# Optimization experiments

Measured on AMD Instinct MI355X. Metric: run time of the kernel, lower is better.

Reference implementation:

```python
import jax, jax.numpy as jnp
import numpy as np

INPUT_DIM = 1024
EMBED_DIM = 1024

def setup_inputs() -> dict:
    key = jax.random.key(0)
    ks = jax.random.split(key, 6)
    B, S = 4, 2048
    q = jax.random.normal(ks[0], (B, S, INPUT_DIM), dtype=jnp.float32)
    k = jax.random.normal(ks[1], (B, S, INPUT_DIM), dtype=jnp.float32)
    v = jax.random.normal(ks[2], (B, S, INPUT_DIM), dtype=jnp.float32)
    # Linear weights stored as [in, out] (y = x @ W), scaled like torch default init
    scale = 1.0 / np.sqrt(INPUT_DIM)
    W_q = jax.random.uniform(ks[3], (INPUT_DIM, EMBED_DIM), jnp.float32, -scale, scale)
    W_k = jax.random.uniform(ks[4], (INPUT_DIM, EMBED_DIM), jnp.float32, -scale, scale)
    W_v = jax.random.uniform(ks[5], (INPUT_DIM, EMBED_DIM), jnp.float32, -scale, scale)
    return {"q": q, "k": k, "v": v, "W_q": W_q, "W_k": W_k, "W_v": W_v}

def reference(q, k, v, W_q, W_k, W_v):
    Q = jnp.einsum('bsd,de->bse', q, W_q)
    K = jnp.einsum('bsd,de->bse', k, W_k)
    V = jnp.einsum('bsd,de->bse', v, W_v)
    scores = jnp.einsum('bqe,bke->bqk', Q, K) / jnp.sqrt(jnp.float32(EMBED_DIM))
    attn = jax.nn.softmax(scores, axis=-1)
    return jnp.einsum('bqk,bke->bqe', attn, V)
```

## Files before the change

### kernel.cpp

```cpp
#include <hip/hip_runtime.h>
#include <math.h>

typedef __attribute__((ext_vector_type(8))) short bfrag;
typedef __attribute__((ext_vector_type(4))) float ffrag;
typedef __attribute__((ext_vector_type(4))) float f4;

__device__ __forceinline__ unsigned short f2bf(float x) {
    unsigned u = __float_as_uint(x);
    return (unsigned short)((u + 0x7fffu + ((u >> 16) & 1u)) >> 16);
}
__device__ __forceinline__ float bf2f(unsigned short h) {
    return __uint_as_float(((unsigned)h) << 16);
}

__device__ __forceinline__ void gload_lds16(const void* g, void* l) {
    __builtin_amdgcn_global_load_lds(
        (const __attribute__((address_space(1))) void*)g,
        (__attribute__((address_space(3))) void*)l,
        16, 0, 0);
}

template<int AMODE, int EPI>
__global__ __launch_bounds__(256)
void gemm_split(const void* __restrict__ Ap, const void* __restrict__ Alp,
                long lda, long strideA,
                const unsigned short* __restrict__ Bhp, const unsigned short* __restrict__ Blp,
                long ldb, long strideB,
                void* __restrict__ Cp, void* __restrict__ Clp,
                long ldc, long strideC,
                int K, float alpha)
{
    __shared__ __align__(16) unsigned short Ash[4096];
    __shared__ __align__(16) unsigned short Asl[4096];
    __shared__ __align__(16) unsigned short Bsh[4096];
    __shared__ __align__(16) unsigned short Bsl[4096];

    const int tid  = threadIdx.x;
    const int lane = tid & 63;
    const int wave = tid >> 6;
    const int wr = wave >> 1, wc = wave & 1;
    const int fr = lane & 15, fq = lane >> 4;
    const long brow = (long)blockIdx.y * 128;
    const long bcol = (long)blockIdx.x * 128;
    const long z = blockIdx.z;

    const unsigned short* Bh = Bhp + z * strideB;
    const unsigned short* Bl = Blp + z * strideB;

    int aoff[4], boff[4];
    #pragma unroll
    for (int m = 0; m < 4; ++m) {
        int rt = wr * 64 + m * 16 + fr;
        aoff[m] = rt * 64 + ((fq ^ ((rt >> 1) & 3)) << 4);
        int ct = wc * 64 + m * 16 + fr;
        boff[m] = ct * 64 + ((fq ^ ((ct >> 1) & 3)) << 4);
    }

    ffrag acc[4][4] = {};

    const int sw_r = lane >> 2;
    const int sw_c = lane & 3;

    for (int k0 = 0; k0 < K; k0 += 32) {
        f4 x0, x1, x2, x3;
        int ar = tid >> 1;
        int kh = (tid & 1) << 4;
        if (AMODE == 0) {
            const float* ap = (const float*)Ap + (brow + ar) * lda + k0 + kh;
            x0 = ((const f4*)ap)[0];
            x1 = ((const f4*)ap)[1];
            x2 = ((const f4*)ap)[2];
            x3 = ((const f4*)ap)[3];
        }
        __syncthreads();

        #pragma unroll
        for (int i = 0; i < 2; ++i) {
            int lin = (wave + i * 4) << 10;
            int rr  = (lin >> 6) + sw_r;
            int cs  = sw_c ^ ((rr >> 1) & 3);
            gload_lds16((const char*)(Bh + (bcol + rr) * ldb + k0) + (cs << 4),
                        (char*)Bsh + lin);
            gload_lds16((const char*)(Bl + (bcol + rr) * ldb + k0) + (cs << 4),
                        (char*)Bsl + lin);
        }
        if (AMODE == 1) {
            const unsigned short* Ah = (const unsigned short*)Ap  + z * strideA;
            const unsigned short* Al = (const unsigned short*)Alp + z * strideA;
            #pragma unroll
            for (int i = 0; i < 2; ++i) {
                int lin = (wave + i * 4) << 10;
                int rr  = (lin >> 6) + sw_r;
                int cs  = sw_c ^ ((rr >> 1) & 3);
                gload_lds16((const char*)(Ah + (brow + rr) * lda + k0) + (cs << 4),
                            (char*)Ash + lin);
                gload_lds16((const char*)(Al + (brow + rr) * lda + k0) + (cs << 4),
                            (char*)Asl + lin);
            }
        } else {
            float xs[16] = {x0.x, x0.y, x0.z, x0.w, x1.x, x1.y, x1.z, x1.w,
                            x2.x, x2.y, x2.z, x2.w, x3.x, x3.y, x3.z, x3.w};
            #pragma unroll
            for (int g = 0; g < 4; ++g) {
                int e = kh + g * 4;
                unsigned short h[4], lo[4];
                #pragma unroll
                for (int j = 0; j < 4; ++j) {
                    float xx = xs[g * 4 + j];
                    h[j]  = f2bf(xx);
                    lo[j] = f2bf(xx - bf2f(h[j]));
                }
                int byte = ar * 64 + (((e >> 3) ^ ((ar >> 1) & 3)) << 4) + ((e & 7) << 1);
                uint2 hv, lv;
                hv.x = (unsigned)h[0]  | ((unsigned)h[1]  << 16);
                hv.y = (unsigned)h[2]  | ((unsigned)h[3]  << 16);
                lv.x = (unsigned)lo[0] | ((unsigned)lo[1] << 16);
                lv.y = (unsigned)lo[2] | ((unsigned)lo[3] << 16);
                *(uint2*)((char*)Ash + byte) = hv;
                *(uint2*)((char*)Asl + byte) = lv;
            }
        }
        __syncthreads();

        bfrag ah[4], alf[4], bh[4], blf[4];
        #pragma unroll
        for (int m = 0; m < 4; ++m) {
            ah[m]  = *(const bfrag*)((const char*)Ash + aoff[m]);
            alf[m] = *(const bfrag*)((const char*)Asl + aoff[m]);
        }
        #pragma unroll
        for (int n = 0; n < 4; ++n) {
            bh[n]  = *(const bfrag*)((const char*)Bsh + boff[n]);
            blf[n] = *(const bfrag*)((const char*)Bsl + boff[n]);
        }
        #pragma unroll
        for (int m = 0; m < 4; ++m)
            #pragma unroll
            for (int n = 0; n < 4; ++n) {
                acc[m][n] = __builtin_amdgcn_mfma_f32_16x16x32_bf16(ah[m],  bh[n],  acc[m][n], 0, 0, 0);
                acc[m][n] = __builtin_amdgcn_mfma_f32_16x16x32_bf16(ah[m],  blf[n], acc[m][n], 0, 0, 0);
                acc[m][n] = __builtin_amdgcn_mfma_f32_16x16x32_bf16(alf[m], bh[n],  acc[m][n], 0, 0, 0);
            }
    }

    if (EPI == 0) {
        float* C = (float*)Cp + z * strideC;
        #pragma unroll
        for (int m = 0; m < 4; ++m) {
            long r0 = brow + wr * 64 + m * 16 + fq * 4;
            #pragma unroll
            for (int n = 0; n < 4; ++n) {
                long c = bcol + wc * 64 + n * 16 + fr;
                #pragma unroll
                for (int j = 0; j < 4; ++j)
                    C[(r0 + j) * ldc + c] = acc[m][n][j] * alpha;
            }
        }
    } else if (EPI == 1) {
        unsigned short* Ch = (unsigned short*)Cp;
        unsigned short* Cl = (unsigned short*)Clp;
        #pragma unroll
        for (int m = 0; m < 4; ++m) {
            long r0 = brow + wr * 64 + m * 16 + fq * 4;
            #pragma unroll
            for (int n = 0; n < 4; ++n) {
                long c = bcol + wc * 64 + n * 16 + fr;
                #pragma unroll
                for (int j = 0; j < 4; ++j) {
                    float xx = acc[m][n][j];
                    unsigned short h = f2bf(xx);
                    Ch[(r0 + j) * ldc + c] = h;
                    Cl[(r0 + j) * ldc + c] = f2bf(xx - bf2f(h));
                }
            }
        }
    } else {
        unsigned short* Ch = (unsigned short*)Cp;
        unsigned short* Cl = (unsigned short*)Clp;
        #pragma unroll
        for (int m = 0; m < 4; ++m) {
            long r0 = brow + wr * 64 + m * 16 + fq * 4;
            long b  = r0 >> 11, sr = r0 & 2047;
            #pragma unroll
            for (int n = 0; n < 4; ++n) {
                long c = bcol + wc * 64 + n * 16 + fr;
                unsigned short h[4], lo[4];
                #pragma unroll
                for (int j = 0; j < 4; ++j) {
                    float xx = acc[m][n][j];
                    h[j]  = f2bf(xx);
                    lo[j] = f2bf(xx - bf2f(h[j]));
                }
                uint2 hv, lv;
                hv.x = (unsigned)h[0]  | ((unsigned)h[1]  << 16);
                hv.y = (unsigned)h[2]  | ((unsigned)h[3]  << 16);
                lv.x = (unsigned)lo[0] | ((unsigned)lo[1] << 16);
                lv.y = (unsigned)lo[2] | ((unsigned)lo[3] << 16);
                *(uint2*)(Ch + (b << 21) + c * 2048 + sr) = hv;
                *(uint2*)(Cl + (b << 21) + c * 2048 + sr) = lv;
            }
        }
    }
}

__global__ __launch_bounds__(256)
void transpose_split(const float* __restrict__ W,
                     unsigned short* __restrict__ Th,
                     unsigned short* __restrict__ Tl)
{
    __shared__ float t[64][65];
    const int tid = threadIdx.x;
    const int d0 = blockIdx.x * 64, e0 = blockIdx.y * 64;
    const int r = tid >> 4, c4 = (tid & 15) * 4;
    #pragma unroll
    for (int i = 0; i < 4; ++i) {
        f4 x = *(const f4*)(W + (long)(d0 + r + i * 16) * 1024 + e0 + c4);
        t[r + i * 16][c4 + 0] = x.x;
        t[r + i * 16][c4 + 1] = x.y;
        t[r + i * 16][c4 + 2] = x.z;
        t[r + i * 16][c4 + 3] = x.w;
    }
    __syncthreads();
    #pragma unroll
    for (int i = 0; i < 4; ++i) {
        int e = r + i * 16;
        unsigned short h[4], lo[4];
        #pragma unroll
        for (int j = 0; j < 4; ++j) {
            float xx = t[c4 + j][e];
            h[j]  = f2bf(xx);
            lo[j] = f2bf(xx - bf2f(h[j]));
        }
        uint2 hv, lv;
        hv.x = (unsigned)h[0]  | ((unsigned)h[1]  << 16);
        hv.y = (unsigned)h[2]  | ((unsigned)h[3]  << 16);
        lv.x = (unsigned)lo[0] | ((unsigned)lo[1] << 16);
        lv.y = (unsigned)lo[2] | ((unsigned)lo[3] << 16);
        long idx = (long)(e0 + e) * 1024 + d0 + c4;
        *(uint2*)(Th + idx) = hv;
        *(uint2*)(Tl + idx) = lv;
    }
}

__global__ __launch_bounds__(256)
void softmax_split(float* __restrict__ Sc)
{
    float* row = Sc + (size_t)blockIdx.x * 2048;
    const int tid = threadIdx.x;
    const int lane = tid & 63, wv = tid >> 6;
    __shared__ float red[8];

    f4 x0 = ((const f4*)row)[tid * 2];
    f4 x1 = ((const f4*)row)[tid * 2 + 1];

    float m = fmaxf(fmaxf(fmaxf(x0.x, x0.y), fmaxf(x0.z, x0.w)),
                    fmaxf(fmaxf(x1.x, x1.y), fmaxf(x1.z, x1.w)));
    #pragma unroll
    for (int o = 32; o > 0; o >>= 1) m = fmaxf(m, __shfl_xor(m, o));
    if (lane == 0) red[wv] = m;
    __syncthreads();
    m = fmaxf(fmaxf(red[0], red[1]), fmaxf(red[2], red[3]));

    float p[8];
    p[0] = __expf(x0.x - m); p[1] = __expf(x0.y - m);
    p[2] = __expf(x0.z - m); p[3] = __expf(x0.w - m);
    p[4] = __expf(x1.x - m); p[5] = __expf(x1.y - m);
    p[6] = __expf(x1.z - m); p[7] = __expf(x1.w - m);

    float s = ((p[0] + p[1]) + (p[2] + p[3])) + ((p[4] + p[5]) + (p[6] + p[7]));
    #pragma unroll
    for (int o = 32; o > 0; o >>= 1) s += __shfl_xor(s, o);
    if (lane == 0) red[4 + wv] = s;
    __syncthreads();
    s = (red[4] + red[5]) + (red[6] + red[7]);

    float inv = 1.0f / s;
    unsigned short h[8], lo[8];
    #pragma unroll
    for (int j = 0; j < 8; ++j) {
        float pv = p[j] * inv;
        h[j]  = f2bf(pv);
        lo[j] = f2bf(pv - bf2f(h[j]));
    }
    uint4 hv, lv;
    hv.x = (unsigned)h[0] | ((unsigned)h[1] << 16);
    hv.y = (unsigned)h[2] | ((unsigned)h[3] << 16);
    hv.z = (unsigned)h[4] | ((unsigned)h[5] << 16);
    hv.w = (unsigned)h[6] | ((unsigned)h[7] << 16);
    lv.x = (unsigned)lo[0] | ((unsigned)lo[1] << 16);
    lv.y = (unsigned)lo[2] | ((unsigned)lo[3] << 16);
    lv.z = (unsigned)lo[4] | ((unsigned)lo[5] << 16);
    lv.w = (unsigned)lo[6] | ((unsigned)lo[7] << 16);
    *(uint4*)((char*)row + tid * 16)        = hv;
    *(uint4*)((char*)row + 4096 + tid * 16) = lv;
}

extern "C" void kernel_launch(void* const* d_in, const int* in_sizes, int n_in,
                              void* d_out, int out_size, void* d_ws, size_t ws_size,
                              hipStream_t stream)
{
    const float* q  = (const float*)d_in[0];
    const float* k  = (const float*)d_in[1];
    const float* v  = (const float*)d_in[2];
    const float* Wq = (const float*)d_in[3];
    const float* Wk = (const float*)d_in[4];
    const float* Wv = (const float*)d_in[5];
    float* out = (float*)d_out;

    const long S = 2048, D = 1024;
    const long SD = S * D;
    const long SS = S * S;

    char* p = (char*)d_ws;
    size_t off = 0;
    unsigned short *WTh[3], *WTl[3];
    for (int i = 0; i < 3; ++i) {
        WTh[i] = (unsigned short*)(p + off); off += (size_t)2 << 20;
        WTl[i] = (unsigned short*)(p + off); off += (size_t)2 << 20;
    }
    unsigned short* Qh  = (unsigned short*)(p + off); off += (size_t)16 << 20;
    unsigned short* Ql  = (unsigned short*)(p + off); off += (size_t)16 << 20;
    unsigned short* Kh  = (unsigned short*)(p + off); off += (size_t)16 << 20;
    unsigned short* Kl  = (unsigned short*)(p + off); off += (size_t)16 << 20;
    unsigned short* VTh = (unsigned short*)(p + off); off += (size_t)16 << 20;
    unsigned short* VTl = (unsigned short*)(p + off); off += (size_t)16 << 20;
    float* Sc = (float*)(p + off);

    size_t avail = (ws_size > off) ? (ws_size - off) : 0;
    int nbat = (avail >= (size_t)64 << 20) ? 4 : ((avail >= (size_t)32 << 20) ? 2 : 1);

    dim3 blk(256);

    transpose_split<<<dim3(16, 16), blk, 0, stream>>>(Wq, WTh[0], WTl[0]);
    transpose_split<<<dim3(16, 16), blk, 0, stream>>>(Wk, WTh[1], WTl[1]);
    transpose_split<<<dim3(16, 16), blk, 0, stream>>>(Wv, WTh[2], WTl[2]);

    gemm_split<0, 1><<<dim3(8, 64, 1), blk, 0, stream>>>(
        q, nullptr, 1024, 0, WTh[0], WTl[0], 1024, 0, Qh, Ql, 1024, 0, 1024, 1.0f);
    gemm_split<0, 1><<<dim3(8, 64, 1), blk, 0, stream>>>(
        k, nullptr, 1024, 0, WTh[1], WTl[1], 1024, 0, Kh, Kl, 1024, 0, 1024, 1.0f);
    gemm_split<0, 2><<<dim3(8, 64, 1), blk, 0, stream>>>(
        v, nullptr, 1024, 0, WTh[2], WTl[2], 1024, 0, VTh, VTl, 0, 0, 1024, 1.0f);

    for (int b0 = 0; b0 < 4; b0 += nbat) {
        int nb = (4 - b0 < nbat) ? (4 - b0) : nbat;
        gemm_split<1, 0><<<dim3(16, 16, nb), blk, 0, stream>>>(
            Qh + b0 * SD, Ql + b0 * SD, 1024, SD,
            Kh + b0 * SD, Kl + b0 * SD, 1024, SD,
            Sc, nullptr, 2048, SS, 1024, 0.03125f);
        softmax_split<<<dim3(2048 * nb), blk, 0, stream>>>(Sc);
        gemm_split<1, 0><<<dim3(8, 16, nb), blk, 0, stream>>>(
            (unsigned short*)Sc, (unsigned short*)Sc + 2048, 4096, 2 * SS,
            VTh + b0 * SD, VTl + b0 * SD, 2048, SD,
            out + b0 * SD, nullptr, 1024, SD, 2048, 1.0f);
    }
}
```

Before: 565.4 us.

## Replace GEMM with 256-row double-buffered 8-wave kernel and pre-split fp32 inputs

Replaces the 128x128 four-wave split-bf16 GEMM with an eight-wave kernel using 256-row tiles. It double-buffers LDS via global_load_lds with explicit vmcnt waits, issues the three split-precision MFMA passes in staged phases overlapping the next tile's loads, raises wave priority, and remaps block IDs for locality. The fp32 projection inputs are now split into hi/lo bf16 by a separate kernel instead of inside the GEMM. This aims to improve MFMA utilization and hide load latency, at the cost of extra workspace, an added elementwise pass over q/k/v, and higher register pressure.

```diff
diff --git a/kernel.cpp b/kernel.cpp
--- a/kernel.cpp
+++ b/kernel.cpp
@@ -5,152 +5,189 @@
 typedef __attribute__((ext_vector_type(4))) float ffrag;
 typedef __attribute__((ext_vector_type(4))) float f4;
 
-__device__ __forceinline__ unsigned short f2bf(float x) {
+static __device__ __forceinline__ unsigned short f2bf(float x) {
     unsigned u = __float_as_uint(x);
     return (unsigned short)((u + 0x7fffu + ((u >> 16) & 1u)) >> 16);
 }
-__device__ __forceinline__ float bf2f(unsigned short h) {
+static __device__ __forceinline__ float bf2f(unsigned short h) {
     return __uint_as_float(((unsigned)h) << 16);
 }
 
-__device__ __forceinline__ void gload_lds16(const void* g, void* l) {
+static __device__ __forceinline__ void gload_lds16(const void* g, void* l) {
     __builtin_amdgcn_global_load_lds(
         (const __attribute__((address_space(1))) void*)g,
         (__attribute__((address_space(3))) void*)l,
         16, 0, 0);
 }
 
-template<int AMODE, int EPI>
-__global__ __launch_bounds__(256)
-void gemm_split(const void* __restrict__ Ap, const void* __restrict__ Alp,
-                long lda, long strideA,
-                const unsigned short* __restrict__ Bhp, const unsigned short* __restrict__ Blp,
-                long ldb, long strideB,
-                void* __restrict__ Cp, void* __restrict__ Clp,
-                long ldc, long strideC,
-                int K, float alpha)
+template<int N> static __device__ __forceinline__ void wait_vm() {
+    asm volatile("s_waitcnt vmcnt(%0)" :: "n"(N) : "memory");
+}
+static __device__ __forceinline__ void lgkm0() {
+    asm volatile("s_waitcnt lgkmcnt(0)" ::: "memory");
+    __builtin_amdgcn_sched_barrier(0);
+}
+
+template<int BN, int EPI>
+__global__ __launch_bounds__(512, 2)
+void gemm8(const unsigned short* __restrict__ Ahp, const unsigned short* __restrict__ Alp,
+           long lda, long strideA,
+           const unsigned short* __restrict__ Bhp, const unsigned short* __restrict__ Blp,
+           long ldb, long strideB,
+           void* __restrict__ Cp, void* __restrict__ Clp,
+           long ldc, long strideC,
+           int K, float alpha, int NXB)
 {
-    __shared__ __align__(16) unsigned short Ash[4096];
-    __shared__ __align__(16) unsigned short Asl[4096];
-    __shared__ __align__(16) unsigned short Bsh[4096];
-    __shared__ __align__(16) unsigned short Bsl[4096];
+    constexpr int NR   = BN / 64;
+    constexpr int LB   = BN / 128;
+    constexpr int LDSA = 16384;
+    constexpr int LDSB = BN * 64;
+    constexpr int G0 = LB + 2;
+    constexpr int G1 = 4 + LB;
+    constexpr int G2 = 2 + 2 * LB;
+
+    __shared__ __align__(16) char smem[4 * LDSA + 4 * LDSB];
 
     const int tid  = threadIdx.x;
     const int lane = tid & 63;
     const int wave = tid >> 6;
-    const int wr = wave >> 1, wc = wave & 1;
+    const int wr = wave >> 2, wc = wave & 3;
     const int fr = lane & 15, fq = lane >> 4;
-    const long brow = (long)blockIdx.y * 128;
-    const long bcol = (long)blockIdx.x * 128;
+
+    int nwg = (int)gridDim.x;
+    int id  = (int)blockIdx.x;
+    id = (id & 7) * (nwg >> 3) + (id >> 3);
+    const int bx = id % NXB, by = id / NXB;
+    const long brow = (long)by * 256;
+    const long bcol = (long)bx * BN;
     const long z = blockIdx.z;
 
-    const unsigned short* Bh = Bhp + z * strideB;
-    const unsigned short* Bl = Blp + z * strideB;
-
-    int aoff[4], boff[4];
-    #pragma unroll
-    for (int m = 0; m < 4; ++m) {
-        int rt = wr * 64 + m * 16 + fr;
+    const char* gAh = (const char*)(Ahp + z * strideA + brow * lda);
+    const char* gAl = (const char*)(Alp + z * strideA + brow * lda);
+    const char* gBh = (const char*)(Bhp + z * strideB + bcol * ldb);
+    const char* gBl = (const char*)(Blp + z * strideB + bcol * ldb);
+
+    int soffA[2], soffB[LB];
+    #pragma unroll
+    for (int j = 0; j < 2; ++j) {
+        int idx = j * 512 + tid, row = idx >> 2;
+        int cs = (tid & 3) ^ ((row >> 1) & 3);
+        soffA[j] = row * (int)(lda * 2) + (cs << 4);
+    }
+    #pragma unroll
+    for (int j = 0; j < LB; ++j) {
+        int idx = j * 512 + tid, row = idx >> 2;
+        int cs = (tid & 3) ^ ((row >> 1) & 3);
+        soffB[j] = row * (int)(ldb * 2) + (cs << 4);
+    }
+
+    int aoff[8], boff[NR];
+    #pragma unroll
+    for (int m = 0; m < 8; ++m) {
+        int rt = wr * 128 + m * 16 + fr;
         aoff[m] = rt * 64 + ((fq ^ ((rt >> 1) & 3)) << 4);
-        int ct = wc * 64 + m * 16 + fr;
-        boff[m] = ct * 64 + ((fq ^ ((ct >> 1) & 3)) << 4);
-    }
-
-    ffrag acc[4][4] = {};
-
-    const int sw_r = lane >> 2;
-    const int sw_c = lane & 3;
-
-    for (int k0 = 0; k0 < K; k0 += 32) {
-        f4 x0, x1, x2, x3;
-        int ar = tid >> 1;
-        int kh = (tid & 1) << 4;
-        if (AMODE == 0) {
-            const float* ap = (const float*)Ap + (brow + ar) * lda + k0 + kh;
-            x0 = ((const f4*)ap)[0];
-            x1 = ((const f4*)ap)[1];
-            x2 = ((const f4*)ap)[2];
-            x3 = ((const f4*)ap)[3];
-        }
-        __syncthreads();
-
-        #pragma unroll
-        for (int i = 0; i < 2; ++i) {
-            int lin = (wave + i * 4) << 10;
-            int rr  = (lin >> 6) + sw_r;
-            int cs  = sw_c ^ ((rr >> 1) & 3);
-            gload_lds16((const char*)(Bh + (bcol + rr) * ldb + k0) + (cs << 4),
-                        (char*)Bsh + lin);
-            gload_lds16((const char*)(Bl + (bcol + rr) * ldb + k0) + (cs << 4),
-                        (char*)Bsl + lin);
-        }
-        if (AMODE == 1) {
-            const unsigned short* Ah = (const unsigned short*)Ap  + z * strideA;
-            const unsigned short* Al = (const unsigned short*)Alp + z * strideA;
-            #pragma unroll
-            for (int i = 0; i < 2; ++i) {
-                int lin = (wave + i * 4) << 10;
-                int rr  = (lin >> 6) + sw_r;
-                int cs  = sw_c ^ ((rr >> 1) & 3);
-                gload_lds16((const char*)(Ah + (brow + rr) * lda + k0) + (cs << 4),
-                            (char*)Ash + lin);
-                gload_lds16((const char*)(Al + (brow + rr) * lda + k0) + (cs << 4),
-                            (char*)Asl + lin);
-            }
-        } else {
-            float xs[16] = {x0.x, x0.y, x0.z, x0.w, x1.x, x1.y, x1.z, x1.w,
-                            x2.x, x2.y, x2.z, x2.w, x3.x, x3.y, x3.z, x3.w};
-            #pragma unroll
-            for (int g = 0; g < 4; ++g) {
-                int e = kh + g * 4;
-                unsigned short h[4], lo[4];
-                #pragma unroll
-                for (int j = 0; j < 4; ++j) {
-                    float xx = xs[g * 4 + j];
-                    h[j]  = f2bf(xx);
-                    lo[j] = f2bf(xx - bf2f(h[j]));
-                }
-                int byte = ar * 64 + (((e >> 3) ^ ((ar >> 1) & 3)) << 4) + ((e & 7) << 1);
-                uint2 hv, lv;
-                hv.x = (unsigned)h[0]  | ((unsigned)h[1]  << 16);
-                hv.y = (unsigned)h[2]  | ((unsigned)h[3]  << 16);
-                lv.x = (unsigned)lo[0] | ((unsigned)lo[1] << 16);
-                lv.y = (unsigned)lo[2] | ((unsigned)lo[3] << 16);
-                *(uint2*)((char*)Ash + byte) = hv;
-                *(uint2*)((char*)Asl + byte) = lv;
-            }
-        }
-        __syncthreads();
-
-        bfrag ah[4], alf[4], bh[4], blf[4];
-        #pragma unroll
-        for (int m = 0; m < 4; ++m) {
-            ah[m]  = *(const bfrag*)((const char*)Ash + aoff[m]);
-            alf[m] = *(const bfrag*)((const char*)Asl + aoff[m]);
-        }
-        #pragma unroll
-        for (int n = 0; n < 4; ++n) {
-            bh[n]  = *(const bfrag*)((const char*)Bsh + boff[n]);
-            blf[n] = *(const bfrag*)((const char*)Bsl + boff[n]);
-        }
-        #pragma unroll
-        for (int m = 0; m < 4; ++m)
-            #pragma unroll
-            for (int n = 0; n < 4; ++n) {
-                acc[m][n] = __builtin_amdgcn_mfma_f32_16x16x32_bf16(ah[m],  bh[n],  acc[m][n], 0, 0, 0);
-                acc[m][n] = __builtin_amdgcn_mfma_f32_16x16x32_bf16(ah[m],  blf[n], acc[m][n], 0, 0, 0);
-                acc[m][n] = __builtin_amdgcn_mfma_f32_16x16x32_bf16(alf[m], bh[n],  acc[m][n], 0, 0, 0);
-            }
-    }
+    }
+    #pragma unroll
+    for (int n = 0; n < NR; ++n) {
+        int ct = wc * (BN / 4) + n * 16 + fr;
+        boff[n] = ct * 64 + ((fq ^ ((ct >> 1) & 3)) << 4);
+    }
+
+    auto stageA = [&](const char* g, char* l, long ko) {
+        #pragma unroll
+        for (int j = 0; j < 2; ++j)
+            gload_lds16(g + ko + soffA[j], l + ((j * 512 + tid) << 4));
+    };
+    auto stageB = [&](const char* g, char* l, long ko) {
+        #pragma unroll
+        for (int j = 0; j < LB; ++j)
+            gload_lds16(g + ko + soffB[j], l + ((j * 512 + tid) << 4));
+    };
+
+    stageB(gBh, smem + 4 * LDSA, 0);
+    stageA(gAh, smem, 0);
+    stageB(gBl, smem + 4 * LDSA + 2 * LDSB, 0);
+    stageA(gAl, smem + 2 * LDSA, 0);
+    wait_vm<G0>();
+    __builtin_amdgcn_s_barrier();
+
+    ffrag acc[8][NR] = {};
+    const int NT = K >> 5;
+
+    for (int t = 0; t < NT; ++t) {
+        const int par = t & 1, parn = par ^ 1;
+        const long ko = (long)(((t + 1) < NT) ? (t + 1) : t) << 6;
+        char* rAh = smem + par * LDSA;
+        char* wAh = smem + parn * LDSA;
+        char* rAl = smem + 2 * LDSA + par * LDSA;
+        char* wAl = smem + 2 * LDSA + parn * LDSA;
+        char* rBh = smem + 4 * LDSA + par * LDSB;
+        char* wBh = smem + 4 * LDSA + parn * LDSB;
+        char* rBl = smem + 4 * LDSA + 2 * LDSB + par * LDSB;
+        char* wBl = smem + 4 * LDSA + 2 * LDSB + parn * LDSB;
+
+        bfrag ah[8], bh[NR];
+        #pragma unroll
+        for (int m = 0; m < 8; ++m) ah[m] = *(const bfrag*)(rAh + aoff[m]);
+        #pragma unroll
+        for (int n = 0; n < NR; ++n) bh[n] = *(const bfrag*)(rBh + boff[n]);
+        stageB(gBh, wBh, ko);
+        stageA(gAh, wAh, ko);
+        __builtin_amdgcn_s_barrier();
+        lgkm0();
+        __builtin_amdgcn_s_setprio(1);
+        #pragma unroll
+        for (int m = 0; m < 8; ++m)
+            #pragma unroll
+            for (int n = 0; n < NR; ++n)
+                acc[m][n] = __builtin_amdgcn_mfma_f32_16x16x32_bf16(ah[m], bh[n], acc[m][n], 0, 0, 0);
+        __builtin_amdgcn_s_setprio(0);
+        wait_vm<G1>();
+        __builtin_amdgcn_s_barrier();
+
+        bfrag bl[NR];
+        #pragma unroll
+        for (int n = 0; n < NR; ++n) bl[n] = *(const bfrag*)(rBl + boff[n]);
+        stageB(gBl, wBl, ko);
+        __builtin_amdgcn_s_barrier();
+        lgkm0();
+        __builtin_amdgcn_s_setprio(1);
+        #pragma unroll
+        for (int m = 0; m < 8; ++m)
+            #pragma unroll
+            for (int n = 0; n < NR; ++n)
+                acc[m][n] = __builtin_amdgcn_mfma_f32_16x16x32_bf16(ah[m], bl[n], acc[m][n], 0, 0, 0);
+        __builtin_amdgcn_s_setprio(0);
+        wait_vm<G2>();
+        __builtin_amdgcn_s_barrier();
+
+        bfrag al[8];
+        #pragma unroll
+        for (int m = 0; m < 8; ++m) al[m] = *(const bfrag*)(rAl + aoff[m]);
+        stageA(gAl, wAl, ko);
+        __builtin_amdgcn_s_barrier();
+        lgkm0();
+        __builtin_amdgcn_s_setprio(1);
+        #pragma unroll
+        for (int m = 0; m < 8; ++m)
+            #pragma unroll
+            for (int n = 0; n < NR; ++n)
+                acc[m][n] = __builtin_amdgcn_mfma_f32_16x16x32_bf16(al[m], bh[n], acc[m][n], 0, 0, 0);
+        __builtin_amdgcn_s_setprio(0);
+        wait_vm<G0>();
+        __builtin_amdgcn_s_barrier();
+    }
+
+    wait_vm<0>();
 
     if (EPI == 0) {
         float* C = (float*)Cp + z * strideC;
         #pragma unroll
-        for (int m = 0; m < 4; ++m) {
-            long r0 = brow + wr * 64 + m * 16 + fq * 4;
-            #pragma unroll
-            for (int n = 0; n < 4; ++n) {
-                long c = bcol + wc * 64 + n * 16 + fr;
+        for (int m = 0; m < 8; ++m) {
+            long r0 = brow + wr * 128 + m * 16 + fq * 4;
+            #pragma unroll
+            for (int n = 0; n < NR; ++n) {
+                long c = bcol + wc * (BN / 4) + n * 16 + fr;
                 #pragma unroll
                 for (int j = 0; j < 4; ++j)
                     C[(r0 + j) * ldc + c] = acc[m][n][j] * alpha;
@@ -160,11 +197,11 @@
         unsigned short* Ch = (unsigned short*)Cp;
         unsigned short* Cl = (unsigned short*)Clp;
         #pragma unroll
-        for (int m = 0; m < 4; ++m) {
-            long r0 = brow + wr * 64 + m * 16 + fq * 4;
-            #pragma unroll
-            for (int n = 0; n < 4; ++n) {
-                long c = bcol + wc * 64 + n * 16 + fr;
+        for (int m = 0; m < 8; ++m) {
+            long r0 = brow + wr * 128 + m * 16 + fq * 4;
+            #pragma unroll
+            for (int n = 0; n < NR; ++n) {
+                long c = bcol + wc * (BN / 4) + n * 16 + fr;
                 #pragma unroll
                 for (int j = 0; j < 4; ++j) {
                     float xx = acc[m][n][j];
@@ -178,12 +215,12 @@
         unsigned short* Ch = (unsigned short*)Cp;
         unsigned short* Cl = (unsigned short*)Clp;
         #pragma unroll
-        for (int m = 0; m < 4; ++m) {
-            long r0 = brow + wr * 64 + m * 16 + fq * 4;
-            long b  = r0 >> 11, sr = r0 & 2047;
-            #pragma unroll
-            for (int n = 0; n < 4; ++n) {
-                long c = bcol + wc * 64 + n * 16 + fr;
+        for (int m = 0; m < 8; ++m) {
+            long r0 = brow + wr * 128 + m * 16 + fq * 4;
+            long b = r0 >> 11, sr = r0 & 2047;
+            #pragma unroll
+            for (int n = 0; n < NR; ++n) {
+                long c = bcol + wc * (BN / 4) + n * 16 + fr;
                 unsigned short h[4], lo[4];
                 #pragma unroll
                 for (int j = 0; j < 4; ++j) {
@@ -204,6 +241,31 @@
 }
 
 __global__ __launch_bounds__(256)
+void split_f32(const float* __restrict__ x, unsigned short* __restrict__ hi,
+               unsigned short* __restrict__ lo, long n4)
+{
+    long i = (long)blockIdx.x * blockDim.x + threadIdx.x;
+    long stride = (long)gridDim.x * blockDim.x;
+    for (; i < n4; i += stride) {
+        f4 v = ((const f4*)x)[i];
+        unsigned short h[4], l[4];
+        #pragma unroll
+        for (int j = 0; j < 4; ++j) {
+            float xx = v[j];
+            h[j] = f2bf(xx);
+            l[j] = f2bf(xx - bf2f(h[j]));
+        }
+        uint2 hv, lv;
+        hv.x = (unsigned)h[0] | ((unsigned)h[1] << 16);
+        hv.y = (unsigned)h[2] | ((unsigned)h[3] << 16);
+        lv.x = (unsigned)l[0] | ((unsigned)l[1] << 16);
+        lv.y = (unsigned)l[2] | ((unsigned)l[3] << 16);
+        ((uint2*)hi)[i] = hv;
+        ((uint2*)lo)[i] = lv;
+    }
+}
+
+__global__ __launch_bounds__(256)
 void transpose_split(const float* __restrict__ W,
                      unsigned short* __restrict__ Th,
                      unsigned short* __restrict__ Tl)
@@ -324,34 +386,42 @@
     unsigned short* Kl  = (unsigned short*)(p + off); off += (size_t)16 << 20;
     unsigned short* VTh = (unsigned short*)(p + off); off += (size_t)16 << 20;
     unsigned short* VTl = (unsigned short*)(p + off); off += (size_t)16 << 20;
-    float* Sc = (float*)(p + off);
-
+    unsigned short* xh  = (unsigned short*)(p + off); off += (size_t)16 << 20;
+    unsigned short* xl  = (unsigned short*)(p + off); off += (size_t)16 << 20;
+
+    float* Sc;
+    int nbat;
     size_t avail = (ws_size > off) ? (ws_size - off) : 0;
-    int nbat = (avail >= (size_t)64 << 20) ? 4 : ((avail >= (size_t)32 << 20) ? 2 : 1);
-
-    dim3 blk(256);
-
-    transpose_split<<<dim3(16, 16), blk, 0, stream>>>(Wq, WTh[0], WTl[0]);
-    transpose_split<<<dim3(16, 16), blk, 0, stream>>>(Wk, WTh[1], WTl[1]);
-    transpose_split<<<dim3(16, 16), blk, 0, stream>>>(Wv, WTh[2], WTl[2]);
-
-    gemm_split<0, 1><<<dim3(8, 64, 1), blk, 0, stream>>>(
-        q, nullptr, 1024, 0, WTh[0], WTl[0], 1024, 0, Qh, Ql, 1024, 0, 1024, 1.0f);
-    gemm_split<0, 1><<<dim3(8, 64, 1), blk, 0, stream>>>(
-        k, nullptr, 1024, 0, WTh[1], WTl[1], 1024, 0, Kh, Kl, 1024, 0, 1024, 1.0f);
-    gemm_split<0, 2><<<dim3(8, 64, 1), blk, 0, stream>>>(
-        v, nullptr, 1024, 0, WTh[2], WTl[2], 1024, 0, VTh, VTl, 0, 0, 1024, 1.0f);
+    if (avail >= (size_t)64 << 20)      { Sc = (float*)(p + off); nbat = 4; }
+    else if (avail >= (size_t)32 << 20) { Sc = (float*)(p + off); nbat = 2; }
+    else                                { Sc = (float*)xh;        nbat = 2; }
+
+    dim3 b256(256), b512(512);
+
+    transpose_split<<<dim3(16, 16), b256, 0, stream>>>(Wq, WTh[0], WTl[0]);
+    transpose_split<<<dim3(16, 16), b256, 0, stream>>>(Wk, WTh[1], WTl[1]);
+    transpose_split<<<dim3(16, 16), b256, 0, stream>>>(Wv, WTh[2], WTl[2]);
+
+    split_f32<<<dim3(2048), b256, 0, stream>>>(q, xh, xl, SD * 4 / 4);
+    gemm8<128, 1><<<dim3(256, 1, 1), b512, 0, stream>>>(
+        xh, xl, 1024, 0, WTh[0], WTl[0], 1024, 0, Qh, Ql, 1024, 0, 1024, 1.0f, 8);
+    split_f32<<<dim3(2048), b256, 0, stream>>>(k, xh, xl, SD * 4 / 4);
+    gemm8<128, 1><<<dim3(256, 1, 1), b512, 0, stream>>>(
+        xh, xl, 1024, 0, WTh[1], WTl[1], 1024, 0, Kh, Kl, 1024, 0, 1024, 1.0f, 8);
+    split_f32<<<dim3(2048), b256, 0, stream>>>(v, xh, xl, SD * 4 / 4);
+    gemm8<128, 2><<<dim3(256, 1, 1), b512, 0, stream>>>(
+        xh, xl, 1024, 0, WTh[2], WTl[2], 1024, 0, VTh, VTl, 0, 0, 1024, 1.0f, 8);
 
     for (int b0 = 0; b0 < 4; b0 += nbat) {
         int nb = (4 - b0 < nbat) ? (4 - b0) : nbat;
-        gemm_split<1, 0><<<dim3(16, 16, nb), blk, 0, stream>>>(
+        gemm8<256, 0><<<dim3(64, 1, nb), b512, 0, stream>>>(
             Qh + b0 * SD, Ql + b0 * SD, 1024, SD,
             Kh + b0 * SD, Kl + b0 * SD, 1024, SD,
-            Sc, nullptr, 2048, SS, 1024, 0.03125f);
-        softmax_split<<<dim3(2048 * nb), blk, 0, stream>>>(Sc);
-        gemm_split<1, 0><<<dim3(8, 16, nb), blk, 0, stream>>>(
+            Sc, nullptr, 2048, SS, 1024, 0.03125f, 8);
+        softmax_split<<<dim3(2048 * nb), b256, 0, stream>>>(Sc);
+        gemm8<128, 0><<<dim3(64, 1, nb), b512, 0, stream>>>(
             (unsigned short*)Sc, (unsigned short*)Sc + 2048, 4096, 2 * SS,
             VTh + b0 * SD, VTl + b0 * SD, 2048, SD,
-            out + b0 * SD, nullptr, 1024, SD, 2048, 1.0f);
-    }
-}
+            out + b0 * SD, nullptr, 1024, SD, 2048, 1.0f, 8);
+    }
+}
```

New measurement: 514.2 us. -9.1%, faster.
